# Performance work log

Measured on AMD Instinct MI355X. Metric: run time of the kernel, lower is better.

## Reference

```python
import jax, jax.numpy as jnp
import numpy as np

K = 3          # deformable conv kernel size
PAD = 1        # padding
BN_EPS = 1e-5


def _upsample2(x):
    # nn.Upsample(scale_factor=2) default mode='nearest' on [B,C,D,H,W]
    x = jnp.repeat(x, 2, axis=2)
    x = jnp.repeat(x, 2, axis=3)
    x = jnp.repeat(x, 2, axis=4)
    return x


def _conv3d(x, w, b):
    out = jax.lax.conv_general_dilated(
        x, w, window_strides=(1, 1, 1), padding=[(PAD, PAD)] * 3,
        dimension_numbers=('NCDHW', 'OIDHW', 'NCDHW'))
    return out + b[None, :, None, None, None]


def _trilinear_sample(x, coords):
    # x: [B,C,D,H,W]; coords: [B,Kt,3,D,H,W] absolute (possibly OOB) positions.
    # Zero padding outside the volume (standard deformable-conv convention).
    B, C, D, H, W = x.shape
    pd, ph, pw = coords[:, :, 0], coords[:, :, 1], coords[:, :, 2]  # [B,Kt,D,H,W]
    d0 = jnp.floor(pd); h0 = jnp.floor(ph); w0 = jnp.floor(pw)
    fd = pd - d0; fh = ph - h0; fw = pw - w0
    x_flat = x.reshape(B, C, D * H * W)

    def gather(di, hi, wi):
        valid = ((di >= 0) & (di < D) & (hi >= 0) & (hi < H) & (wi >= 0) & (wi < W))
        dc = jnp.clip(di, 0, D - 1).astype(jnp.int32)
        hc = jnp.clip(hi, 0, H - 1).astype(jnp.int32)
        wc = jnp.clip(wi, 0, W - 1).astype(jnp.int32)
        flat = (dc * H + hc) * W + wc                       # [B,Kt,D,H,W]
        vals = jax.vmap(lambda xf, idx: jnp.take(xf, idx.reshape(-1), axis=1))(x_flat, flat)
        vals = vals.reshape(B, C, *flat.shape[1:])          # [B,C,Kt,D,H,W]
        return vals * valid[:, None].astype(x.dtype)

    out = jnp.zeros((B, C) + pd.shape[1:], x.dtype)
    for dd in (0, 1):
        for hh in (0, 1):
            for ww in (0, 1):
                wgt = ((fd if dd else 1.0 - fd)
                       * (fh if hh else 1.0 - fh)
                       * (fw if ww else 1.0 - fw))           # [B,Kt,D,H,W]
                out = out + gather(d0 + dd, h0 + hh, w0 + ww) * wgt[:, None]
    return out  # [B,C,Kt,D,H,W]


def _deform_conv3d(x, w_off, b_off, w, b):
    B, C, D, H, W = x.shape
    Kt = K ** 3
    # offsets: Conv3d(C, 3*K^3, k=3, pad=1) -> [B, Kt, 3(dz,dy,dx), D,H,W]
    off = _conv3d(x, w_off, b_off).reshape(B, Kt, 3, D, H, W)
    # kernel tap displacements relative to output voxel: [Kt,3]
    taps = jnp.stack(jnp.meshgrid(jnp.arange(K), jnp.arange(K), jnp.arange(K),
                                  indexing='ij'), -1).reshape(-1, 3).astype(x.dtype) - PAD
    grid = jnp.stack(jnp.meshgrid(jnp.arange(D, dtype=x.dtype),
                                  jnp.arange(H, dtype=x.dtype),
                                  jnp.arange(W, dtype=x.dtype),
                                  indexing='ij'), 0)          # [3,D,H,W]
    coords = grid[None, None] + taps[None, :, :, None, None, None] + off  # [B,Kt,3,D,H,W]
    sampled = _trilinear_sample(x, coords)                    # [B,C,Kt,D,H,W]
    out = jnp.einsum('bckdhw,ock->bodhw', sampled, w.reshape(w.shape[0], C, Kt))
    return out + b[None, :, None, None, None]


def setup_inputs() -> dict:
    key = jax.random.key(0)
    ks = jax.random.split(key, 4)
    ch_in, ch_out = 64, 32
    x = jax.random.normal(ks[0], (1, ch_in, 16, 16, 16), jnp.float32)
    w_off = jax.random.normal(ks[1], (3 * K ** 3, ch_in, K, K, K), jnp.float32) * 0.01
    b_off = jnp.zeros((3 * K ** 3,), jnp.float32)
    w = jax.random.normal(ks[2], (ch_out, ch_in, K, K, K), jnp.float32) * 0.05
    b = jnp.zeros((ch_out,), jnp.float32)
    gamma = jnp.ones((ch_out,), jnp.float32)
    beta = jnp.zeros((ch_out,), jnp.float32)
    return {"x": x, "w_off": w_off, "b_off": b_off, "w": w, "b": b,
            "gamma": gamma, "beta": beta}


def reference(x, w_off, b_off, w, b, gamma, beta):
    x = _upsample2(x)                                  # [B,C,2D,2H,2W]
    out = _deform_conv3d(x, w_off, b_off, w, b)        # [B,ch_out,2D,2H,2W]
    # BatchNorm3d (training-mode batch stats) + ReLU
    mean = out.mean(axis=(0, 2, 3, 4), keepdims=True)
    var = out.var(axis=(0, 2, 3, 4), keepdims=True)
    out = (out - mean) * jax.lax.rsqrt(var + BN_EPS)
    out = out * gamma[None, :, None, None, None] + beta[None, :, None, None, None]
    return jax.nn.relu(out)
```

## Files before the change

### kernel.cpp

```cpp
#include <hip/hip_runtime.h>
#include <math.h>

#define NVOX  32768
#define CIN   64
#define COUT  32
#define KT    27
#define CIT   1728
#define PSP   5832

#define WS_XT   0
#define WS_WA   186624
#define WS_WO   214272
#define WS_STAT 297216

typedef __attribute__((ext_vector_type(8))) _Float16 half8;
typedef __attribute__((ext_vector_type(2))) _Float16 half2v;
typedef __attribute__((ext_vector_type(4))) float floatx4;

static __device__ __forceinline__ unsigned dup16(float w) {
    unsigned short b = __builtin_bit_cast(unsigned short, (_Float16)w);
    return (unsigned)b * 0x10001u;
}
static __device__ __forceinline__ half2v u2h2(unsigned u) {
    return __builtin_bit_cast(half2v, u);
}
static __device__ __forceinline__ half8 pk8(half2v a, half2v b, half2v c, half2v d) {
    union { half8 v; half2v p[4]; } u;
    u.p[0] = a; u.p[1] = b; u.p[2] = c; u.p[3] = d;
    return u.v;
}

__global__ __launch_bounds__(256) void prep_all_kernel(
        const float* __restrict__ x, const float* __restrict__ w_off,
        const float* __restrict__ wmat, float* __restrict__ ws) {
    int b = blockIdx.x, t = threadIdx.x;
    if (b < 92) {
        __shared__ _Float16 tile[64][65];
        _Float16* xth = (_Float16*)(ws + WS_XT);
        int tq = t >> 6, lane = t & 63;
        int base = b * 64;
        int cell = base + lane;
        int qw = cell % 18, qh = (cell / 18) % 18, qd = cell / 324;
        bool interior = (cell < PSP) && qd >= 1 && qd <= 16 && qh >= 1 && qh <= 16
                        && qw >= 1 && qw <= 16;
        int xbase = interior ? (((qd - 1) * 16 + (qh - 1)) * 16 + (qw - 1)) : 0;
#pragma unroll
        for (int i = 0; i < 16; i++) {
            int c = tq * 16 + i;
            float v = interior ? x[c * 4096 + xbase] : 0.f;
            tile[lane][c] = (_Float16)v;
        }
        __syncthreads();
#pragma unroll
        for (int i = 0; i < 16; i++) {
            int s = tq * 16 + i;
            int cell2 = base + s;
            if (cell2 < PSP) xth[cell2 * 64 + lane] = tile[s][lane];
        }
    } else if (b < 119) {
        _Float16* wa = (_Float16*)(ws + WS_WA);
        int idx = (b - 92) * 256 + t;
        int kb = idx >> 5, o = idx & 31;
        half8 r;
#pragma unroll
        for (int j = 0; j < 8; j++) {
            int kk = kb * 8 + j;
            int tap = kk >> 6, ci = kk & 63;
            r[j] = (_Float16)wmat[o * CIT + ci * 27 + tap];
        }
        *(half8*)(wa + idx * 8) = r;
    } else if (b < 200) {
        _Float16* wo = (_Float16*)(ws + WS_WO);
        int idx = (b - 119) * 256 + t;
        int kb = idx / 96, m = idx % 96;
        half8 r;
#pragma unroll
        for (int j = 0; j < 8; j++) {
            int kk = kb * 8 + j;
            int tap = kk >> 6, ci = kk & 63;
            float v = (m < 81) ? w_off[(m * 64 + ci) * 27 + tap] : 0.f;
            r[j] = (_Float16)v;
        }
        *(half8*)(wo + idx * 8) = r;
    } else {
        if (t < 64) ws[WS_STAT + t] = 0.f;
    }
}

#define ACCP(xl, xh, Wx) do { \
    s00 += (Wx) * u2h2((unsigned)(xl).x); s01 += (Wx) * u2h2((unsigned)(xl).y); \
    s02 += (Wx) * u2h2((unsigned)(xl).z); s03 += (Wx) * u2h2((unsigned)(xl).w); \
    s10 += (Wx) * u2h2((unsigned)(xh).x); s11 += (Wx) * u2h2((unsigned)(xh).y); \
    s12 += (Wx) * u2h2((unsigned)(xh).z); s13 += (Wx) * u2h2((unsigned)(xh).w); \
} while (0)

#define DO2(ap, wp) do { \
    int a0_ = (ap) & 0x7fff, a1_ = (int)((((unsigned)(ap)) >> 16) & 0x7fffu); \
    unsigned wl_ = ((unsigned)(wp) & 0xffffu) * 0x10001u; \
    unsigned wh_ = (((unsigned)(wp)) >> 16) * 0x10001u; \
    int4 x0l_ = *(const int4*)(region + (a0_ ^ subLo)); \
    int4 x0h_ = *(const int4*)(region + (a0_ ^ subHi)); \
    int4 x1l_ = *(const int4*)(region + (a1_ ^ subLo)); \
    int4 x1h_ = *(const int4*)(region + (a1_ ^ subHi)); \
    ACCP(x0l_, x0h_, u2h2(wl_)); ACCP(x1l_, x1h_, u2h2(wh_)); \
} while (0)

#define GSLOW(Ax, wf) do { \
    half2v Wq_ = u2h2(dup16(wf)); \
    int4 xl_ = *(const int4*)(xtb + (Ax) + subLo); \
    int4 xh_ = *(const int4*)(xtb + (Ax) + subLo + 64); \
    t00 += Wq_ * u2h2((unsigned)xl_.x); t01 += Wq_ * u2h2((unsigned)xl_.y); \
    t02 += Wq_ * u2h2((unsigned)xl_.z); t03 += Wq_ * u2h2((unsigned)xl_.w); \
    t10 += Wq_ * u2h2((unsigned)xh_.x); t11 += Wq_ * u2h2((unsigned)xh_.y); \
    t12 += Wq_ * u2h2((unsigned)xh_.z); t13 += Wq_ * u2h2((unsigned)xh_.w); \
} while (0)

__global__ __launch_bounds__(256, 4) void fused_kernel(
        const float* __restrict__ b_off, const float* __restrict__ bias,
        float* ws, float* __restrict__ out) {
    __shared__ __align__(16) char shmem[34816];
    char* region = shmem;
    int2* scratch2 = (int2*)(shmem + 25600);
    _Float16* Pl = (_Float16*)(shmem + 28672);
    float* pbuf = (float*)shmem;
    float* rsumS = (float*)(shmem + 8704);
    float* rsqS  = (float*)(shmem + 8832);

    int tid = threadIdx.x, wave = tid >> 6, lane = tid & 63;
    int col = lane & 15, quad = lane >> 4;
    int bid = blockIdx.x;
    int d0 = (bid >> 6) << 1, h0 = ((bid >> 2) & 15) << 1, w0 = (bid & 3) << 3;

    const char* xtb = (const char*)(ws + WS_XT);
    const half8* wa8 = (const half8*)(ws + WS_WA);
    float* gstat = ws + WS_STAT;

    {
        int4* ab4 = (int4*)shmem;
        const _Float16* abuf16 = (const _Float16*)shmem;
        const int4* wsrc = (const int4*)(ws + WS_WO);
        int nsub = wave & 1, mh = wave >> 1;
        int vv = nsub * 16 + col;
        int dA = d0 + (vv >> 4), hA = h0 + ((vv >> 3) & 1), wA = w0 + (vv & 7);

        int4 ra0 = wsrc[tid], ra1 = wsrc[256 + tid], ra2 = wsrc[512 + tid];
        ab4[tid] = ra0; ab4[256 + tid] = ra1; ab4[512 + tid] = ra2;
        ra0 = wsrc[768 + tid]; ra1 = wsrc[768 + 256 + tid]; ra2 = wsrc[768 + 512 + tid];

        int c0;
        {
            int rd = ((dA - 1) >> 1) + 1, rh = ((hA - 1) >> 1) + 1, rw = ((wA - 1) >> 1) + 1;
            c0 = (rd * 18 + rh) * 18 + rw;
        }
        int4 bx0 = *(const int4*)(xtb + c0 * 128 + quad * 16);
        int4 bx1 = *(const int4*)(xtb + c0 * 128 + 64 + quad * 16);
        __syncthreads();

        floatx4 oacc[3];
#pragma unroll
        for (int mt = 0; mt < 3; mt++) oacc[mt] = (floatx4){0.f, 0.f, 0.f, 0.f};

#pragma unroll 1
        for (int tap = 0; tap < 27; tap++) {
            if (tap < 26) {
                int4* dst = ab4 + ((tap + 1) & 1) * 768;
                dst[tid] = ra0; dst[256 + tid] = ra1; dst[512 + tid] = ra2;
            }
            if (tap < 25) {
                const int4* s2 = wsrc + (tap + 2) * 768;
                ra0 = s2[tid]; ra1 = s2[256 + tid]; ra2 = s2[512 + tid];
            }
            int4 nbx0 = bx0, nbx1 = bx1;
            if (tap < 26) {
                int tn = tap + 1;
                int kd = tn / 9, r9 = tn - kd * 9, kh2 = r9 / 3, kw2 = r9 - kh2 * 3;
                int rd = ((dA + kd - 1) >> 1) + 1;
                int rh = ((hA + kh2 - 1) >> 1) + 1;
                int rw = ((wA + kw2 - 1) >> 1) + 1;
                int nc = (rd * 18 + rh) * 18 + rw;
                nbx0 = *(const int4*)(xtb + nc * 128 + quad * 16);
                nbx1 = *(const int4*)(xtb + nc * 128 + 64 + quad * 16);
            }
            const _Float16* abh = abuf16 + (tap & 1) * 6144;
            half8 bf0 = __builtin_bit_cast(half8, bx0);
            half8 bf1 = __builtin_bit_cast(half8, bx1);
#pragma unroll
            for (int mt = 0; mt < 3; mt++) {
                half8 a0 = *(const half8*)(abh + quad * 768 + (mh * 48 + mt * 16 + col) * 8);
                oacc[mt] = __builtin_amdgcn_mfma_f32_16x16x32_f16(a0, bf0, oacc[mt], 0, 0, 0);
            }
#pragma unroll
            for (int mt = 0; mt < 3; mt++) {
                half8 a1 = *(const half8*)(abh + (4 + quad) * 768 + (mh * 48 + mt * 16 + col) * 8);
                oacc[mt] = __builtin_amdgcn_mfma_f32_16x16x32_f16(a1, bf1, oacc[mt], 0, 0, 0);
            }
            bx0 = nbx0; bx1 = nbx1;
            __syncthreads();
        }

#pragma unroll
        for (int mt = 0; mt < 3; mt++)
#pragma unroll
            for (int r = 0; r < 4; r++) {
                int m = mh * 48 + mt * 16 + quad * 4 + r;
                if (m < 81)
                    Pl[m * 32 + vv] = (_Float16)(oacc[mt][r] + b_off[m]);
            }
        __syncthreads();
    }

    int pdlo = (d0 >> 1) - 1, phlo = (h0 >> 1) - 1, pwlo = (w0 >> 1) - 1;

#pragma unroll 1
    for (int it = 0; it < 7; it++) {
        int i = it * 256 + tid;
        if (i < 1600) {
            int r = i >> 3, c16 = i & 7;
            int rd = r / 40, rem = r - rd * 40, rh = rem >> 3, rw = rem & 7;
            int pd = min(max(pdlo + rd, 0), 17);
            int ph = min(max(phlo + rh, 0), 17);
            int pw = min(max(pwlo + rw, 0), 17);
            int cell = (pd * 18 + ph) * 18 + pw;
            int4 vsrc = *(const int4*)(xtb + cell * 128 + c16 * 16);
            int f = (r ^ (r >> 3)) & 7;
            *(int4*)(region + r * 128 + ((c16 ^ f) << 4)) = vsrc;
        }
    }
    __syncthreads();

    int vh = wave & 1, kt = wave >> 1;
    int v = vh * 16 + col;
    int dv = v >> 4, hv = (v >> 3) & 1, wv = v & 7;
    int dcoord = d0 + dv, hcoord = h0 + hv, wcoord = w0 + wv;
    int gvox = dcoord * 1024 + hcoord * 32 + wcoord;
    int tbeg = kt ? 14 : 0, tend = kt ? 27 : 14;
    int subLo = quad * 16, subHi = subLo + 64;
    int bd = quad >> 1, bh = quad & 1;

    floatx4 acc0 = {0.f, 0.f, 0.f, 0.f}, acc1 = {0.f, 0.f, 0.f, 0.f};

    float od = (float)Pl[(3 * tbeg + 0) * 32 + v];
    float oh = (float)Pl[(3 * tbeg + 1) * 32 + v];
    float ow = (float)Pl[(3 * tbeg + 2) * 32 + v];

#pragma unroll 1
    for (int tap = tbeg; tap < tend; tap++) {
        int kd = tap / 9, r9 = tap - kd * 9, kh2 = r9 / 3, kw2 = r9 - kh2 * 3;
        float pdc = (float)(dcoord + kd - 1) + od;
        float phc = (float)(hcoord + kh2 - 1) + oh;
        float pwc = (float)(wcoord + kw2 - 1) + ow;
        float fd0 = floorf(pdc), fh0 = floorf(phc), fw0 = floorf(pwc);
        float fd = pdc - fd0, fh = phc - fh0, fw = pwc - fw0;
        int id = (int)fd0, ih = (int)fh0, iw = (int)fw0;

        int cd0 = ((min(max(id,     -2), 33)) >> 1) + 1;
        int cd1 = ((min(max(id + 1, -2), 33)) >> 1) + 1;
        int ch0 = ((min(max(ih,     -2), 33)) >> 1) + 1;
        int ch1 = ((min(max(ih + 1, -2), 33)) >> 1) + 1;
        int cw0 = ((min(max(iw,     -2), 33)) >> 1) + 1;
        int cw1 = ((min(max(iw + 1, -2), 33)) >> 1) + 1;
        int sd0 = cd0 - pdlo, sd1 = cd1 - pdlo;
        int sh0 = ch0 - phlo, sh1 = ch1 - phlo;
        int sw0 = cw0 - pwlo, sw1 = cw1 - pwlo;
        bool oob = ((unsigned)sd0 > 4u) | ((unsigned)sd1 > 4u)
                 | ((unsigned)sh0 > 4u) | ((unsigned)sh1 > 4u)
                 | ((unsigned)sw0 > 7u) | ((unsigned)sw1 > 7u);

        int sdq = bd ? sd1 : sd0, shq = bh ? sh1 : sh0;
        int rb = (sdq * 5 + shq) * 8;
        int r0 = rb + sw0, r1 = rb + sw1;
        int f0 = (r0 ^ (r0 >> 3)) & 7, f1 = (r1 ^ (r1 >> 3)) & 7;
        int a0 = oob ? 0x8000 : ((r0 << 7) | (f0 << 4));
        int a1 = oob ? 0x8000 : ((r1 << 7) | (f1 << 4));
        float gdw = 1.f - fd, ghw = 1.f - fh, gww = 1.f - fw;
        float wd = bd ? fd : gdw, wh = bh ? fh : ghw;
        float wdh = wd * wh;
        unsigned wb0 = (unsigned)__builtin_bit_cast(unsigned short, (_Float16)(wdh * gww));
        unsigned wb1 = (unsigned)__builtin_bit_cast(unsigned short, (_Float16)(wdh * fw));
        scratch2[(wave * 16 + col) * 6 + quad] =
            make_int2(a0 | (a1 << 16), (int)(wb0 | (wb1 << 16)));

        if (tap + 1 < tend) {
            od = (float)Pl[(3 * tap + 3) * 32 + v];
            oh = (float)Pl[(3 * tap + 4) * 32 + v];
            ow = (float)Pl[(3 * tap + 5) * 32 + v];
        }

        int kb = tap * 8 + quad;
        half8 a00 = wa8[kb * 32 + col];
        half8 a01 = wa8[kb * 32 + 16 + col];
        half8 a10 = wa8[(kb + 4) * 32 + col];
        half8 a11 = wa8[(kb + 4) * 32 + 16 + col];

        const int4* sc = (const int4*)(scratch2 + (wave * 16 + col) * 6);
        int4 p0 = sc[0], p1 = sc[1];

        half2v s00 = {0, 0}, s01 = {0, 0}, s02 = {0, 0}, s03 = {0, 0};
        half2v s10 = {0, 0}, s11 = {0, 0}, s12 = {0, 0}, s13 = {0, 0};
        DO2(p0.x, p0.y); DO2(p0.z, p0.w);
        DO2(p1.x, p1.y); DO2(p1.z, p1.w);

        if (__any((p0.x & 0x8000) != 0)) {
            bool flg = (p0.x & 0x8000) != 0;
            int Rd0 = ((min(max(id,     -2), 33) >> 1) + 1) * (324 * 128);
            int Rd1 = ((min(max(id + 1, -2), 33) >> 1) + 1) * (324 * 128);
            int Rh0 = ((min(max(ih,     -2), 33) >> 1) + 1) * (18 * 128);
            int Rh1 = ((min(max(ih + 1, -2), 33) >> 1) + 1) * (18 * 128);
            int Rw0 = ((min(max(iw,     -2), 33) >> 1) + 1) * 128;
            int Rw1 = ((min(max(iw + 1, -2), 33) >> 1) + 1) * 128;
            half2v t00 = {0,0}, t01 = {0,0}, t02 = {0,0}, t03 = {0,0};
            half2v t10 = {0,0}, t11 = {0,0}, t12 = {0,0}, t13 = {0,0};
            GSLOW(Rd0 + Rh0 + Rw0, gdw * ghw * gww);
            GSLOW(Rd0 + Rh0 + Rw1, gdw * ghw * fw);
            GSLOW(Rd0 + Rh1 + Rw0, gdw * fh  * gww);
            GSLOW(Rd0 + Rh1 + Rw1, gdw * fh  * fw);
            GSLOW(Rd1 + Rh0 + Rw0, fd  * ghw * gww);
            GSLOW(Rd1 + Rh0 + Rw1, fd  * ghw * fw);
            GSLOW(Rd1 + Rh1 + Rw0, fd  * fh  * gww);
            GSLOW(Rd1 + Rh1 + Rw1, fd  * fh  * fw);
            s00 = flg ? t00 : s00; s01 = flg ? t01 : s01;
            s02 = flg ? t02 : s02; s03 = flg ? t03 : s03;
            s10 = flg ? t10 : s10; s11 = flg ? t11 : s11;
            s12 = flg ? t12 : s12; s13 = flg ? t13 : s13;
        }

        half8 bf0 = pk8(s00, s01, s02, s03);
        half8 bf1 = pk8(s10, s11, s12, s13);

        acc0 = __builtin_amdgcn_mfma_f32_16x16x32_f16(a00, bf0, acc0, 0, 0, 0);
        acc1 = __builtin_amdgcn_mfma_f32_16x16x32_f16(a01, bf0, acc1, 0, 0, 0);
        acc0 = __builtin_amdgcn_mfma_f32_16x16x32_f16(a10, bf1, acc0, 0, 0, 0);
        acc1 = __builtin_amdgcn_mfma_f32_16x16x32_f16(a11, bf1, acc1, 0, 0, 0);
    }

    __syncthreads();
    if (kt == 1) {
#pragma unroll
        for (int r = 0; r < 4; r++) {
            pbuf[((vh * 2 + 0) * 16 + quad * 4 + r) * 17 + col] = acc0[r];
            pbuf[((vh * 2 + 1) * 16 + quad * 4 + r) * 17 + col] = acc1[r];
        }
    }
    if (tid < 64) ((float*)(shmem + 8704))[tid] = 0.f;
    __syncthreads();
    if (kt == 0) {
#pragma unroll
        for (int r = 0; r < 4; r++) {
            int i = quad * 4 + r;
            int o0 = i;
            float v0 = acc0[r] + pbuf[((vh * 2 + 0) * 16 + i) * 17 + col] + bias[o0];
            out[o0 * NVOX + gvox] = v0;
            atomicAdd(&rsumS[o0], v0);
            atomicAdd(&rsqS[o0], v0 * v0);
            int o1 = 16 + i;
            float v1 = acc1[r] + pbuf[((vh * 2 + 1) * 16 + i) * 17 + col] + bias[o1];
            out[o1 * NVOX + gvox] = v1;
            atomicAdd(&rsumS[o1], v1);
            atomicAdd(&rsqS[o1], v1 * v1);
        }
    }
    __syncthreads();
    if (tid < COUT) {
        atomicAdd(&gstat[tid], rsumS[tid]);
        atomicAdd(&gstat[COUT + tid], rsqS[tid]);
    }
}

__global__ void bn_kernel(const float* __restrict__ ws,
                          const float* __restrict__ gamma,
                          const float* __restrict__ beta,
                          float* out) {
    int i = blockIdx.x * 256 + threadIdx.x;
    int o = i >> 15;
    const float* gstat = ws + WS_STAT;
    const float inv = 1.f / 32768.f;
    float mean = gstat[o] * inv;
    float var  = gstat[COUT + o] * inv - mean * mean;
    float sc   = rsqrtf(var + 1e-5f) * gamma[o];
    float v = (out[i] - mean) * sc + beta[o];
    out[i] = fmaxf(v, 0.f);
}

extern "C" void kernel_launch(void* const* d_in, const int* in_sizes, int n_in,
                              void* d_out, int out_size, void* d_ws, size_t ws_size,
                              hipStream_t stream) {
    const float* x     = (const float*)d_in[0];
    const float* w_off = (const float*)d_in[1];
    const float* b_off = (const float*)d_in[2];
    const float* wmat  = (const float*)d_in[3];
    const float* bias  = (const float*)d_in[4];
    const float* gamma = (const float*)d_in[5];
    const float* beta  = (const float*)d_in[6];
    float* ws  = (float*)d_ws;
    float* out = (float*)d_out;

    prep_all_kernel<<<201, 256, 0, stream>>>(x, w_off, wmat, ws);
    fused_kernel<<<1024, 256, 0, stream>>>(b_off, bias, ws, out);
    bn_kernel<<<4096, 256, 0, stream>>>(ws, gamma, beta, out);
}
```

Before: 145.1 us.

## Fuse BatchNorm+ReLU into main kernel via software grid barrier

Removes the separate BN kernel. Each block keeps its conv outputs in registers, adds its partial statistics to global sums, then waits at an atomic grid-wide barrier (counter zeroed in the prep kernel). After the barrier it reads the final stats and writes normalized, ReLU'd outputs directly. This saves one kernel launch and a full read-modify-write pass over the output. It relies on all 1024 blocks being resident at once; if they are not, the kernel deadlocks, and the spin-wait adds a synchronization tail.

```diff
diff --git a/kernel.cpp b/kernel.cpp
--- a/kernel.cpp
+++ b/kernel.cpp
@@ -12,6 +12,7 @@
 #define WS_WA   186624
 #define WS_WO   214272
 #define WS_STAT 297216
+#define WS_BAR  297280
 
 typedef __attribute__((ext_vector_type(8))) _Float16 half8;
 typedef __attribute__((ext_vector_type(2))) _Float16 half2v;
@@ -83,7 +84,7 @@
         }
         *(half8*)(wo + idx * 8) = r;
     } else {
-        if (t < 64) ws[WS_STAT + t] = 0.f;
+        if (t < 66) ws[WS_STAT + t] = 0.f;
     }
 }
 
@@ -115,8 +116,9 @@
     t12 += Wq_ * u2h2((unsigned)xh_.z); t13 += Wq_ * u2h2((unsigned)xh_.w); \
 } while (0)
 
-__global__ __launch_bounds__(256, 4) void fused_kernel(
+__global__ __launch_bounds__(256, 4) void mega_kernel(
         const float* __restrict__ b_off, const float* __restrict__ bias,
+        const float* __restrict__ gamma, const float* __restrict__ beta,
         float* ws, float* __restrict__ out) {
     __shared__ __align__(16) char shmem[34816];
     char* region = shmem;
@@ -343,20 +345,17 @@
     }
     if (tid < 64) ((float*)(shmem + 8704))[tid] = 0.f;
     __syncthreads();
+    float v0[4] = {0.f, 0.f, 0.f, 0.f}, v1[4] = {0.f, 0.f, 0.f, 0.f};
     if (kt == 0) {
 #pragma unroll
         for (int r = 0; r < 4; r++) {
             int i = quad * 4 + r;
-            int o0 = i;
-            float v0 = acc0[r] + pbuf[((vh * 2 + 0) * 16 + i) * 17 + col] + bias[o0];
-            out[o0 * NVOX + gvox] = v0;
-            atomicAdd(&rsumS[o0], v0);
-            atomicAdd(&rsqS[o0], v0 * v0);
-            int o1 = 16 + i;
-            float v1 = acc1[r] + pbuf[((vh * 2 + 1) * 16 + i) * 17 + col] + bias[o1];
-            out[o1 * NVOX + gvox] = v1;
-            atomicAdd(&rsumS[o1], v1);
-            atomicAdd(&rsqS[o1], v1 * v1);
+            v0[r] = acc0[r] + pbuf[((vh * 2 + 0) * 16 + i) * 17 + col] + bias[i];
+            atomicAdd(&rsumS[i], v0[r]);
+            atomicAdd(&rsqS[i], v0[r] * v0[r]);
+            v1[r] = acc1[r] + pbuf[((vh * 2 + 1) * 16 + i) * 17 + col] + bias[16 + i];
+            atomicAdd(&rsumS[16 + i], v1[r]);
+            atomicAdd(&rsqS[16 + i], v1[r] * v1[r]);
         }
     }
     __syncthreads();
@@ -364,21 +363,37 @@
         atomicAdd(&gstat[tid], rsumS[tid]);
         atomicAdd(&gstat[COUT + tid], rsqS[tid]);
     }
-}
-
-__global__ void bn_kernel(const float* __restrict__ ws,
-                          const float* __restrict__ gamma,
-                          const float* __restrict__ beta,
-                          float* out) {
-    int i = blockIdx.x * 256 + threadIdx.x;
-    int o = i >> 15;
-    const float* gstat = ws + WS_STAT;
-    const float inv = 1.f / 32768.f;
-    float mean = gstat[o] * inv;
-    float var  = gstat[COUT + o] * inv - mean * mean;
-    float sc   = rsqrtf(var + 1e-5f) * gamma[o];
-    float v = (out[i] - mean) * sc + beta[o];
-    out[i] = fmaxf(v, 0.f);
+    __syncthreads();
+
+    if (tid == 0) {
+        unsigned* bar = (unsigned*)(ws + WS_BAR);
+        __hip_atomic_fetch_add(bar, 1u, __ATOMIC_ACQ_REL, __HIP_MEMORY_SCOPE_AGENT);
+        while (__hip_atomic_load(bar, __ATOMIC_ACQUIRE, __HIP_MEMORY_SCOPE_AGENT) < 1024u)
+            __builtin_amdgcn_s_sleep(8);
+    }
+    __syncthreads();
+
+    float* stats = (float*)shmem;
+    if (tid < 64)
+        stats[tid] = __hip_atomic_load(ws + WS_STAT + tid, __ATOMIC_RELAXED,
+                                       __HIP_MEMORY_SCOPE_AGENT);
+    __syncthreads();
+    if (kt == 0) {
+        const float inv = 1.f / 32768.f;
+#pragma unroll
+        for (int r = 0; r < 4; r++) {
+            int i = quad * 4 + r;
+            int o0 = i, o1 = 16 + i;
+            float m0 = stats[o0] * inv;
+            float var0 = stats[32 + o0] * inv - m0 * m0;
+            float sc0 = rsqrtf(var0 + 1e-5f) * gamma[o0];
+            out[o0 * NVOX + gvox] = fmaxf((v0[r] - m0) * sc0 + beta[o0], 0.f);
+            float m1 = stats[o1] * inv;
+            float var1 = stats[32 + o1] * inv - m1 * m1;
+            float sc1 = rsqrtf(var1 + 1e-5f) * gamma[o1];
+            out[o1 * NVOX + gvox] = fmaxf((v1[r] - m1) * sc1 + beta[o1], 0.f);
+        }
+    }
 }
 
 extern "C" void kernel_launch(void* const* d_in, const int* in_sizes, int n_in,
@@ -395,6 +410,5 @@
     float* out = (float*)d_out;
 
     prep_all_kernel<<<201, 256, 0, stream>>>(x, w_off, wmat, ws);
-    fused_kernel<<<1024, 256, 0, stream>>>(b_off, bias, ws, out);
-    bn_kernel<<<4096, 256, 0, stream>>>(ws, gamma, beta, out);
-}
+    mega_kernel<<<1024, 256, 0, stream>>>(b_off, bias, gamma, beta, ws, out);
+}
```

Result: slower. 279.6 us (+92.6%).
